# Kernel optimization log

Hardware: AMD Instinct MI355X
Metric: run time of the kernel (lower is better)

Reference implementation:

```python
import jax, jax.numpy as jnp
import numpy as np

V, H, T, B, S = 50000, 256, 32, 64, 512


def setup_inputs() -> dict:
    key = jax.random.key(0)
    ks = jax.random.split(key, 16)
    sc = 0.05
    def n(k, shape):
        return jax.random.normal(k, shape, dtype=jnp.float32) * sc
    return {
        "seq": jax.random.randint(ks[0], (B, S), 0, V),
        "mask": jnp.ones((B, S), dtype=jnp.int32),
        "labels": jax.random.randint(ks[1], (B, S), 0, T),
        "embedding": n(ks[2], (V, H)),
        "Wih_f": n(ks[3], (4 * H, H)), "Whh_f": n(ks[4], (4 * H, H)),
        "bih_f": n(ks[5], (4 * H,)), "bhh_f": n(ks[6], (4 * H,)),
        "Wih_b": n(ks[7], (4 * H, H)), "Whh_b": n(ks[8], (4 * H, H)),
        "bih_b": n(ks[9], (4 * H,)), "bhh_b": n(ks[10], (4 * H,)),
        "fcW": n(ks[11], (T, 2 * H)), "fcb": n(ks[12], (T,)),
        "start_trans": n(ks[13], (T,)), "end_trans": n(ks[14], (T,)),
        "trans": n(ks[15], (T, T)),
    }


def _lstm_dir(x, Wih, Whh, bih, bhh, reverse):
    # x: [S,B,H]; torch LSTM gate order i,f,g,o
    Bz, Hh = x.shape[1], Whh.shape[1]
    def step(carry, xt):
        h, c = carry
        g = xt @ Wih.T + h @ Whh.T + bih + bhh  # [B,4H]
        i, f, gg, o = jnp.split(g, 4, axis=-1)
        c = jax.nn.sigmoid(f) * c + jax.nn.sigmoid(i) * jnp.tanh(gg)
        h = jax.nn.sigmoid(o) * jnp.tanh(c)
        return (h, c), h
    init = (jnp.zeros((Bz, Hh), x.dtype), jnp.zeros((Bz, Hh), x.dtype))
    _, hs = jax.lax.scan(step, init, x, reverse=reverse)
    return hs


def _crf_llh(em, tags, mask, start, end, trans):
    # em [S,B,T], tags [S,B] int, mask [S,B] bool -> scalar sum log-likelihood
    Sx, Bx, Tx = em.shape
    barange = jnp.arange(Bx)
    em_sc = jnp.take_along_axis(em, tags[:, :, None], axis=2)[..., 0]  # [S,B]
    m = mask.astype(em.dtype)
    num = start[tags[0]] + em_sc[0]
    tr_sc = trans[tags[:-1], tags[1:]]  # [S-1,B]
    num = num + jnp.sum((tr_sc + em_sc[1:]) * m[1:], axis=0)
    seq_ends = jnp.sum(mask.astype(jnp.int32), axis=0) - 1
    last_tags = tags[seq_ends, barange]
    num = num + end[last_tags]
    # forward algorithm (log-partition)
    def step(score, em_m):
        em_t, m_t = em_m
        nxt = jax.nn.logsumexp(score[:, :, None] + trans[None], axis=1) + em_t
        return jnp.where(m_t[:, None], nxt, score), None
    score0 = start[None] + em[0]
    score, _ = jax.lax.scan(step, score0, (em[1:], mask[1:]))
    den = jax.nn.logsumexp(score + end[None], axis=1)
    return jnp.sum(num - den)


def _viterbi(em, mask, start, end, trans):
    Sx, Bx, Tx = em.shape
    def step(score, em_m):
        em_t, m_t = em_m
        cand = score[:, :, None] + trans[None]  # [B,T_prev,T_cur]
        idx = jnp.argmax(cand, axis=1)
        nxt = jnp.max(cand, axis=1) + em_t
        idx = jnp.where(m_t[:, None], idx, jnp.arange(Tx)[None])
        return jnp.where(m_t[:, None], nxt, score), idx
    score0 = start[None] + em[0]
    score, hist = jax.lax.scan(step, score0, (em[1:], mask[1:]))  # hist [S-1,B,T]
    last = jnp.argmax(score + end[None], axis=1)  # [B]
    barange = jnp.arange(Bx)
    def back(tag, idx_t):
        prev = idx_t[barange, tag]
        return prev, prev
    _, prevs = jax.lax.scan(back, last, hist, reverse=True)  # prevs[k] = tag at time k
    return jnp.concatenate([prevs, last[None]], axis=0)  # [S,B]


def reference(seq, mask, labels, embedding, Wih_f, Whh_f, bih_f, bhh_f,
              Wih_b, Whh_b, bih_b, bhh_b, fcW, fcb,
              start_trans, end_trans, trans):
    x = seq.T  # [S,B] time-major as in original
    emb = embedding[x]  # [S,B,H]
    hf = _lstm_dir(emb, Wih_f, Whh_f, bih_f, bhh_f, False)
    hb = _lstm_dir(emb, Wih_b, Whh_b, bih_b, bhh_b, True)
    out = jnp.concatenate([hf, hb], axis=-1)  # [S,B,2H]
    logits = out @ fcW.T + fcb  # [S,B,T]; dropout is identity at eval
    m = mask.T.astype(bool)  # [S,B]
    loss = -_crf_llh(logits, labels.T, m, start_trans, end_trans, trans)
    preds = _viterbi(logits, m, start_trans, end_trans, trans)  # [S,B]
    return preds.T, loss
```

## Files before the change

kernel.cpp:

```cpp
#include <hip/hip_runtime.h>
#include <stdint.h>

#define SS 512
#define BB 64
#define HH 256
#define TT 32

typedef __attribute__((ext_vector_type(8))) short bf16x8;
typedef __attribute__((ext_vector_type(4))) short short4v;
typedef __attribute__((ext_vector_type(4))) float f32x4;
typedef __attribute__((ext_vector_type(8))) int i32x8;
typedef __attribute__((ext_vector_type(4))) int i32x4;

__device__ __forceinline__ unsigned short f2bf(float f){
  unsigned u = __float_as_uint(f);
  unsigned r = (u + 0x7FFFu + ((u >> 16) & 1u)) >> 16;
  return (unsigned short)r;
}
__device__ __forceinline__ float bf2f(unsigned short s){
  return __uint_as_float(((unsigned)s) << 16);
}
__device__ __forceinline__ float sigm(float x){ return 1.0f/(1.0f+__expf(-x)); }
__device__ __forceinline__ float ftanh(float x){
  float e = __expf(2.f*x);
  return 1.f - 2.f/(e + 1.f);
}
__device__ __forceinline__ unsigned cvt4fp8(float a0, float a1, float a2, float a3){
  int d = __builtin_amdgcn_cvt_pk_fp8_f32(a0, a1, 0, false);
  d = __builtin_amdgcn_cvt_pk_fp8_f32(a2, a3, d, true);
  return (unsigned)d;
}
__device__ __forceinline__ unsigned short cvt2fp8(float a0, float a1){
  int d = __builtin_amdgcn_cvt_pk_fp8_f32(a0, a1, 0, false);
  return (unsigned short)(d & 0xFFFF);
}

__device__ __forceinline__ bf16x8 afrag(const unsigned short* A, int mt, int ktp, int nl, int kq){
  int m = mt*16 + nl;
  int sw = (m & 7) << 3;
  int kk = ktp*32 + kq*4;
  short4v lo = *(const short4v*)(A + (m << 8) + (kk ^ sw));
  short4v hi = *(const short4v*)(A + (m << 8) + ((kk + 16) ^ sw));
  bf16x8 r = {lo[0],lo[1],lo[2],lo[3],hi[0],hi[1],hi[2],hi[3]};
  return r;
}

__global__ __launch_bounds__(256,1) void k_xgemm(
    const int* __restrict__ seq, const float* __restrict__ emb,
    const float* __restrict__ Wih_f, const float* __restrict__ Wih_b,
    const float* __restrict__ bih_f, const float* __restrict__ bhh_f,
    const float* __restrict__ bih_b, const float* __restrict__ bhh_b,
    unsigned short* __restrict__ gx)
{
  __shared__ __align__(16) unsigned short A_l[128*256];
  __shared__ __align__(16) unsigned short B_l[64*256];

  const int tid = threadIdx.x;
  const int lane = tid & 63, w = tid >> 6;
  const int nl = lane & 15, kq = lane >> 4;
  const int pbase = blockIdx.x * 128;
  const int dir = blockIdx.y;
  const float* Wih  = dir ? Wih_b : Wih_f;
  const float* bihd = dir ? bih_b : bih_f;
  const float* bhhd = dir ? bhh_b : bhh_f;

#pragma unroll
  for (int i = 0; i < 16; ++i){
    int c = tid + i*256;
    int m = c >> 5, k8 = c & 31;
    int p = pbase + m, t = p >> 6, b = p & 63;
    int er = seq[b*SS + t];
    const float* s = emb + (size_t)er*HH + k8*8;
    float4 x0 = *(const float4*)s, x1 = *(const float4*)(s+4);
    union { unsigned short u[8]; uint4 v; } o;
    o.u[0]=f2bf(x0.x); o.u[1]=f2bf(x0.y); o.u[2]=f2bf(x0.z); o.u[3]=f2bf(x0.w);
    o.u[4]=f2bf(x1.x); o.u[5]=f2bf(x1.y); o.u[6]=f2bf(x1.z); o.u[7]=f2bf(x1.w);
    *(uint4*)&A_l[(m << 8) + ((k8*8) ^ ((m & 7) << 3))] = o.v;
  }

  for (int nb = 0; nb < 16; ++nb){
    __syncthreads();
#pragma unroll
    for (int i = 0; i < 8; ++i){
      int c = tid + i*256;
      int m = c >> 5, k8 = c & 31;
      const float* s = Wih + (size_t)(nb*64 + m)*HH + k8*8;
      float4 x0 = *(const float4*)s, x1 = *(const float4*)(s+4);
      union { unsigned short u[8]; uint4 v; } o;
      o.u[0]=f2bf(x0.x); o.u[1]=f2bf(x0.y); o.u[2]=f2bf(x0.z); o.u[3]=f2bf(x0.w);
      o.u[4]=f2bf(x1.x); o.u[5]=f2bf(x1.y); o.u[6]=f2bf(x1.z); o.u[7]=f2bf(x1.w);
      *(uint4*)&B_l[(m << 8) + ((k8*8) ^ ((m & 7) << 3))] = o.v;
    }
    __syncthreads();

    f32x4 acc[2][4];
#pragma unroll
    for (int mt = 0; mt < 2; ++mt)
#pragma unroll
      for (int nt = 0; nt < 4; ++nt) acc[mt][nt] = (f32x4){0.f,0.f,0.f,0.f};

#pragma unroll
    for (int kt = 0; kt < 8; ++kt){
      bf16x8 a0 = afrag(A_l, w*2+0, kt, nl, kq);
      bf16x8 a1 = afrag(A_l, w*2+1, kt, nl, kq);
#pragma unroll
      for (int nt = 0; nt < 4; ++nt){
        bf16x8 bv = afrag(B_l, nt, kt, nl, kq);
        acc[0][nt] = __builtin_amdgcn_mfma_f32_16x16x32_bf16(a0, bv, acc[0][nt], 0,0,0);
        acc[1][nt] = __builtin_amdgcn_mfma_f32_16x16x32_bf16(a1, bv, acc[1][nt], 0,0,0);
      }
    }

#pragma unroll
    for (int mt = 0; mt < 2; ++mt)
#pragma unroll
      for (int nt = 0; nt < 4; ++nt){
        int p0 = pbase + w*32 + mt*16 + kq*4;
        int t = p0 >> 6, b0 = p0 & 63;
        int col = nb*64 + nt*16 + nl;
        float bs = bihd[col] + bhhd[col];
        union { unsigned short u[4]; uint2 v; } o;
        o.u[0]=f2bf(acc[mt][nt][0] + bs); o.u[1]=f2bf(acc[mt][nt][1] + bs);
        o.u[2]=f2bf(acc[mt][nt][2] + bs); o.u[3]=f2bf(acc[mt][nt][3] + bs);
        *(uint2*)(gx + ((size_t)(dir*16 + (b0 >> 2))*SS + t)*4096 + col*4) = o.v;
      }
  }
}

#define WSC 64.0f
#define HSC 16.0f
#define ISC (1.0f/(WSC*HSC))

__global__ __launch_bounds__(1024,1) void k_lstm(
    const unsigned short* __restrict__ gx,
    const float* __restrict__ Whh_f, const float* __restrict__ Whh_b,
    unsigned short* __restrict__ hf, unsigned short* __restrict__ hb)
{
  __shared__ __align__(16) unsigned char h8[2][16][272];
  __shared__ __align__(16) float xch[16][4][16][4];

  const int tid  = threadIdx.x;
  const int lane = tid & 63;
  const int w    = tid >> 6;
  const int nl   = lane & 15;
  const int kq   = lane >> 4;
  const int dir  = blockIdx.x >> 4;
  const int bg   = blockIdx.x & 15;

  const float* Whh = dir ? Whh_b : Whh_f;
  unsigned short* hbuf = dir ? hb : hf;
  const unsigned short* gxd = gx + (size_t)(dir*16 + bg)*SS*4096;

  i32x8 wB[4][2];
#pragma unroll
  for (int g = 0; g < 4; ++g)
#pragma unroll
    for (int inst = 0; inst < 2; ++inst){
      int ncol = g*256 + w*16 + nl;
      i32x8 bfrag;
#pragma unroll
      for (int d = 0; d < 8; ++d){
        int k0 = inst*128 + kq*32 + d*4;
        float4 v = *(const float4*)(Whh + (size_t)ncol*HH + k0);
        bfrag[d] = (int)cvt4fp8(v.x*WSC, v.y*WSC, v.z*WSC, v.w*WSC);
      }
      wB[g][inst] = bfrag;
    }

  const int cc = w*16 + nl;

  for (int i = tid; i < 2176; i += 1024) ((unsigned*)h8)[i] = 0;
  __syncthreads();

  float c0 = 0.f;

  const int aoff = nl*272 + kq*32;
  const int woff = kq*272 + w*16 + nl;
  const ptrdiff_t gstep = dir ? -4096 : 4096;
  const unsigned short* gbase = gxd + (size_t)(dir ? (SS-1) : 0)*4096 + cc*4 + kq;
  unsigned short* hstore = hbuf + (size_t)(dir ? (SS-1) : 1)*BB*HH + (size_t)(bg*4 + kq)*HH + cc;
  const ptrdiff_t hstep = (dir ? -(ptrdiff_t)1 : (ptrdiff_t)1)*BB*HH;

  unsigned short gxc[4], gxn[4];
#pragma unroll
  for (int g = 0; g < 4; ++g) gxc[g] = gbase[g*1024];

  for (int s = 0; s < SS; ++s){
    const unsigned short* gnext = (s + 1 < SS) ? (gbase + gstep) : gbase;
#pragma unroll
    for (int g = 0; g < 4; ++g) gxn[g] = gnext[g*1024];

    const unsigned char* tp8 = &h8[s & 1][0][0] + aoff;
    i32x8 af0, af1;
    {
      i32x4 lo = *(const i32x4*)(tp8);
      i32x4 hi = *(const i32x4*)(tp8 + 16);
      af0 = (i32x8){lo[0],lo[1],lo[2],lo[3],hi[0],hi[1],hi[2],hi[3]};
      i32x4 lo2 = *(const i32x4*)(tp8 + 128);
      i32x4 hi2 = *(const i32x4*)(tp8 + 144);
      af1 = (i32x8){lo2[0],lo2[1],lo2[2],lo2[3],hi2[0],hi2[1],hi2[2],hi2[3]};
    }

    f32x4 acc[4];
#pragma unroll
    for (int g = 0; g < 4; ++g) acc[g] = (f32x4){0.f,0.f,0.f,0.f};

#pragma unroll
    for (int g = 0; g < 4; ++g)
      acc[g] = __builtin_amdgcn_mfma_scale_f32_16x16x128_f8f6f4(
                 af0, wB[g][0], acc[g], 0, 0, 0, 0x7F7F7F7F, 0, 0x7F7F7F7F);
#pragma unroll
    for (int g = 0; g < 4; ++g)
      acc[g] = __builtin_amdgcn_mfma_scale_f32_16x16x128_f8f6f4(
                 af1, wB[g][1], acc[g], 0, 0, 0, 0x7F7F7F7F, 0, 0x7F7F7F7F);

    if (kq == 0){
#pragma unroll
      for (int g = 0; g < 4; ++g)
        *(f32x4*)&xch[w][g][nl][0] = acc[g];
    }
    asm volatile("s_waitcnt lgkmcnt(0)" ::: "memory");

    {
      float i_ = xch[w][0][nl][kq]*ISC + bf2f(gxc[0]);
      float f_ = xch[w][1][nl][kq]*ISC + bf2f(gxc[1]);
      float g_ = xch[w][2][nl][kq]*ISC + bf2f(gxc[2]);
      float o_ = xch[w][3][nl][kq]*ISC + bf2f(gxc[3]);
      float cn = sigm(f_)*c0 + sigm(i_)*ftanh(g_);
      c0 = cn;
      float h = sigm(o_)*ftanh(cn);

      float s1 = __shfl_xor(h, 1);
      unsigned short p01 = cvt2fp8(h*HSC, s1*HSC);
      unsigned p23 = __shfl_xor((unsigned)p01, 2);
      if ((nl & 3) == 0){
        unsigned word = (unsigned)p01 | (p23 << 16);
        *(unsigned*)(&h8[(s + 1) & 1][0][0] + woff) = word;
      }
      if (!(nl & 1)){
        unsigned hv;
        asm volatile("v_cvt_pk_bf16_f32 %0, %1, %2" : "=v"(hv) : "v"(h), "v"(s1));
        *(unsigned*)hstore = hv;
      }
    }

#pragma unroll
    for (int g = 0; g < 4; ++g) gxc[g] = gxn[g];
    gbase = gnext;
    hstore += hstep;

    asm volatile("s_waitcnt lgkmcnt(0)" ::: "memory");
    __builtin_amdgcn_s_barrier();
    asm volatile("" ::: "memory");
  }
}

__global__ __launch_bounds__(256,1) void k_fc(
    const unsigned short* __restrict__ hf, const unsigned short* __restrict__ hb,
    const float* __restrict__ fcW, const float* __restrict__ fcb,
    float* __restrict__ logits)
{
  __shared__ unsigned short Bs[32][516];
  __shared__ unsigned short Ah[4][32][260];
  __shared__ float fcb_s[32];
  const int tid = threadIdx.x;
  for (int i = tid; i < 32*512; i += 256){
    int tg = i >> 9, k = i & 511;
    Bs[tg][k] = f2bf(fcW[tg*512 + k]);
  }
  if (tid < 32) fcb_s[tid] = fcb[tid];
  __syncthreads();

  const int lane = tid & 63, w = tid >> 6;
  const int nl = lane & 15, kq = lane >> 4;
  const int pbase = blockIdx.x * 128;

  f32x4 acc[2][2];
#pragma unroll
  for (int mt = 0; mt < 2; ++mt)
#pragma unroll
    for (int nt = 0; nt < 2; ++nt) acc[mt][nt] = (f32x4){0.f,0.f,0.f,0.f};

  for (int half = 0; half < 2; ++half){
    for (int rr = 0; rr < 32; ++rr){
      int p = pbase + w*32 + rr;
      int t = p >> 6, b = p & 63;
      const unsigned short* src = half ? (hb + (size_t)(t*BB + b)*HH)
                                       : (hf + (size_t)((t+1)*BB + b)*HH);
      *(uint2*)&Ah[w][rr][lane*4] = *(const uint2*)(src + lane*4);
    }
#pragma unroll
    for (int kt = 0; kt < 8; ++kt){
      int kl = kt*32 + kq*4;
      bf16x8 a[2];
#pragma unroll
      for (int mt = 0; mt < 2; ++mt){
        const unsigned short* ar = &Ah[w][mt*16 + nl][kl];
        short4v lo = *(const short4v*)ar;
        short4v hi = *(const short4v*)(ar + 16);
        bf16x8 f = {lo[0],lo[1],lo[2],lo[3],hi[0],hi[1],hi[2],hi[3]};
        a[mt] = f;
      }
#pragma unroll
      for (int nt = 0; nt < 2; ++nt){
        const unsigned short* br = &Bs[nt*16 + nl][half*256 + kl];
        short4v lo = *(const short4v*)br;
        short4v hi = *(const short4v*)(br + 16);
        bf16x8 bv = {lo[0],lo[1],lo[2],lo[3],hi[0],hi[1],hi[2],hi[3]};
        acc[0][nt] = __builtin_amdgcn_mfma_f32_16x16x32_bf16(a[0], bv, acc[0][nt], 0,0,0);
        acc[1][nt] = __builtin_amdgcn_mfma_f32_16x16x32_bf16(a[1], bv, acc[1][nt], 0,0,0);
      }
    }
  }
#pragma unroll
  for (int mt = 0; mt < 2; ++mt)
#pragma unroll
    for (int nt = 0; nt < 2; ++nt)
#pragma unroll
      for (int r = 0; r < 4; ++r){
        int p = pbase + w*32 + mt*16 + kq*4 + r;
        int tg = nt*16 + nl;
        logits[(size_t)p*TT + tg] = acc[mt][nt][r] + fcb_s[tg];
      }
}

__global__ void k_crf(const float* __restrict__ logits, const int* __restrict__ mask,
                      const int* __restrict__ labels,
                      const float* __restrict__ start, const float* __restrict__ endt,
                      const float* __restrict__ trans,
                      float* __restrict__ den, float* __restrict__ num,
                      float* __restrict__ preds)
{
  __shared__ float tr[1024];
  __shared__ unsigned char vh_l[4][SS-1][32];
  const int tid = threadIdx.x;
  const int role = blockIdx.x >> 4;
  const int bq   = blockIdx.x & 15;
  if (role != 2){
    for (int i = tid; i < 1024; i += 256) tr[i] = trans[i];
    __syncthreads();
  }
  const int lane = tid & 63, w = tid >> 6;
  const int b = bq*4 + w;
  const int grp = lane >> 5, tp = lane & 31;

  if (role == 0){
    float score = start[tp] + logits[(size_t)b*TT + tp];
    float em_c = logits[(size_t)(BB + b)*TT + tp];
    int   mk_c = mask[b*SS + 1];
    for (int s = 1; s < SS; ++s){
      int sn = (s + 1 < SS) ? s + 1 : s;
      float em_n = logits[(size_t)(sn*BB + b)*TT + tp];
      int   mk_n = mask[b*SS + sn];
      float m = -1e30f;
#pragma unroll
      for (int jj = 0; jj < 16; ++jj){
        int j = grp*16 + jj;
        float v = __shfl(score, j) + tr[j*32 + tp];
        m = fmaxf(m, v);
      }
      m = fmaxf(m, __shfl_xor(m, 32));
      float ssum = 0.f;
#pragma unroll
      for (int jj = 0; jj < 16; ++jj){
        int j = grp*16 + jj;
        float v = __shfl(score, j) + tr[j*32 + tp];
        ssum += __expf(v - m);
      }
      ssum += __shfl_xor(ssum, 32);
      float ns = m + __logf(ssum) + em_c;
      score = mk_c ? ns : score;
      em_c = em_n; mk_c = mk_n;
    }
    float v = score + endt[tp];
    float mm = v;
    for (int d = 1; d < 32; d <<= 1) mm = fmaxf(mm, __shfl_xor(mm, d));
    float se = __expf(v - mm);
    for (int d = 1; d < 32; d <<= 1) se += __shfl_xor(se, d);
    if (lane == 0) den[b] = mm + __logf(se);
  } else if (role == 1){
    float score = start[tp] + logits[(size_t)b*TT + tp];
    float em_c = logits[(size_t)(BB + b)*TT + tp];
    int   mk_c = mask[b*SS + 1];
    for (int s = 1; s < SS; ++s){
      int sn = (s + 1 < SS) ? s + 1 : s;
      float em_n = logits[(size_t)(sn*BB + b)*TT + tp];
      int   mk_n = mask[b*SS + sn];
      float m = -1e30f; int am = 0;
#pragma unroll
      for (int jj = 0; jj < 16; ++jj){
        int j = grp*16 + jj;
        float v = __shfl(score, j) + tr[j*32 + tp];
        if (v > m){ m = v; am = j; }
      }
      float om = __shfl_xor(m, 32); int oam = __shfl_xor(am, 32);
      if (om > m || (om == m && oam < am)){ m = om; am = oam; }
      float ns = m + em_c;
      int idx = mk_c ? am : tp;
      if (grp == 0) vh_l[w][s-1][tp] = (unsigned char)idx;
      score = mk_c ? ns : score;
      em_c = em_n; mk_c = mk_n;
    }
    float v = score + endt[tp]; int a = tp;
    for (int d = 1; d < 32; d <<= 1){
      float ov = __shfl_xor(v, d); int oa = __shfl_xor(a, d);
      if (ov > v || (ov == v && oa < a)){ v = ov; a = oa; }
    }
    int tag = __shfl(a, 0);
    if (lane == 0) preds[(size_t)b*SS + SS - 1] = (float)tag;
    for (int s = SS - 1; s >= 1; --s){
      int rv = vh_l[w][s-1][tp];
      int pv = __shfl(rv, tag);
      if (lane == 0) preds[(size_t)b*SS + s - 1] = (float)pv;
      tag = pv;
    }
  } else {
    float acc = 0.f; int mcnt = 0;
    for (int s = lane; s < SS; s += 64){
      int mk = mask[b*SS + s];
      mcnt += mk;
      if (s >= 1){
        int tg = labels[b*SS + s], tpp = labels[b*SS + s - 1];
        float v = trans[tpp*32 + tg] + logits[(size_t)(s*BB + b)*TT + tg];
        acc += mk ? v : 0.f;
      }
    }
    for (int d = 1; d < 64; d <<= 1){ acc += __shfl_xor(acc, d); mcnt += __shfl_xor(mcnt, d); }
    if (lane == 0){
      int t0 = labels[b*SS];
      int tl = labels[b*SS + (mcnt - 1)];
      num[b] = start[t0] + logits[(size_t)b*TT + t0] + acc + endt[tl];
    }
  }
}

__global__ void k_loss(const float* __restrict__ num, const float* __restrict__ den,
                       float* __restrict__ out)
{
  int l = threadIdx.x;
  float v = num[l] - den[l];
  for (int d = 1; d < 64; d <<= 1) v += __shfl_xor(v, d);
  if (l == 0) out[BB*SS] = -v;
}

extern "C" void kernel_launch(void* const* d_in, const int* in_sizes, int n_in,
                              void* d_out, int out_size, void* d_ws, size_t ws_size,
                              hipStream_t stream)
{
  const int*   seq       = (const int*)  d_in[0];
  const int*   mask      = (const int*)  d_in[1];
  const int*   labels    = (const int*)  d_in[2];
  const float* embedding = (const float*)d_in[3];
  const float* Wih_f     = (const float*)d_in[4];
  const float* Whh_f     = (const float*)d_in[5];
  const float* bih_f     = (const float*)d_in[6];
  const float* bhh_f     = (const float*)d_in[7];
  const float* Wih_b     = (const float*)d_in[8];
  const float* Whh_b     = (const float*)d_in[9];
  const float* bih_b     = (const float*)d_in[10];
  const float* bhh_b     = (const float*)d_in[11];
  const float* fcW       = (const float*)d_in[12];
  const float* fcb       = (const float*)d_in[13];
  const float* start_t   = (const float*)d_in[14];
  const float* end_t     = (const float*)d_in[15];
  const float* trans     = (const float*)d_in[16];

  char* ws = (char*)d_ws;
  size_t off = 0;
  unsigned short* gxb = (unsigned short*)(ws + off); off += (size_t)2*SS*1024*64*2;
  unsigned short* hf  = (unsigned short*)(ws + off); off += (size_t)(SS+1)*BB*HH*2;
  unsigned short* hb  = (unsigned short*)(ws + off); off += (size_t)(SS+1)*BB*HH*2;
  float*          lgt = (float*)(ws + off);          off += (size_t)SS*BB*TT*4;
  float*          den = (float*)(ws + off);          off += 256;
  float*          num = (float*)(ws + off);          off += 256;

  k_xgemm<<<dim3(256,2), 256, 0, stream>>>(seq, embedding, Wih_f, Wih_b,
                                           bih_f, bhh_f, bih_b, bhh_b, gxb);
  k_lstm<<<32, 1024, 0, stream>>>(gxb, Whh_f, Whh_b, hf, hb);
  k_fc<<<256, 256, 0, stream>>>(hf, hb, fcW, fcb, lgt);
  k_crf<<<48, 256, 0, stream>>>(lgt, mask, labels, start_t, end_t, trans, den, num, (float*)d_out);
  k_loss<<<1, 64, 0, stream>>>(num, den, (float*)d_out);
}
```

Before: 1.385 ms.

## Fuse input GEMM and LSTM recurrence into one kernel with flag-based overlap

Merges the input-projection GEMM and the recurrent LSTM into a single launch. The first 32 blocks run the recurrence, and the remaining blocks compute gate pre-activations in time order, publishing per-tile completion flags through atomics. LSTM blocks poll these flags before consuming each timestep, so the serial recurrence can start while the GEMM is still running instead of waiting for a full separate kernel. This relies on the GEMM blocks actually being scheduled alongside the resident LSTM blocks. It also adds atomic loads, polling with a guard counter, and an extra memset launch.

```diff
diff --git a/kernel.cpp b/kernel.cpp
--- a/kernel.cpp
+++ b/kernel.cpp
@@ -45,111 +45,114 @@
   return r;
 }
 
-__global__ __launch_bounds__(256,1) void k_xgemm(
+#define WSC 64.0f
+#define HSC 16.0f
+#define ISC (1.0f/(WSC*HSC))
+
+__global__ __launch_bounds__(1024,1) void k_fused(
     const int* __restrict__ seq, const float* __restrict__ emb,
     const float* __restrict__ Wih_f, const float* __restrict__ Wih_b,
     const float* __restrict__ bih_f, const float* __restrict__ bhh_f,
     const float* __restrict__ bih_b, const float* __restrict__ bhh_b,
-    unsigned short* __restrict__ gx)
+    const float* __restrict__ Whh_f, const float* __restrict__ Whh_b,
+    unsigned short* __restrict__ gx,
+    unsigned short* __restrict__ hf, unsigned short* __restrict__ hb,
+    unsigned int* flags)
 {
-  __shared__ __align__(16) unsigned short A_l[128*256];
-  __shared__ __align__(16) unsigned short B_l[64*256];
-
-  const int tid = threadIdx.x;
-  const int lane = tid & 63, w = tid >> 6;
-  const int nl = lane & 15, kq = lane >> 4;
-  const int pbase = blockIdx.x * 128;
-  const int dir = blockIdx.y;
-  const float* Wih  = dir ? Wih_b : Wih_f;
-  const float* bihd = dir ? bih_b : bih_f;
-  const float* bhhd = dir ? bhh_b : bhh_f;
-
-#pragma unroll
-  for (int i = 0; i < 16; ++i){
-    int c = tid + i*256;
-    int m = c >> 5, k8 = c & 31;
-    int p = pbase + m, t = p >> 6, b = p & 63;
-    int er = seq[b*SS + t];
-    const float* s = emb + (size_t)er*HH + k8*8;
-    float4 x0 = *(const float4*)s, x1 = *(const float4*)(s+4);
-    union { unsigned short u[8]; uint4 v; } o;
-    o.u[0]=f2bf(x0.x); o.u[1]=f2bf(x0.y); o.u[2]=f2bf(x0.z); o.u[3]=f2bf(x0.w);
-    o.u[4]=f2bf(x1.x); o.u[5]=f2bf(x1.y); o.u[6]=f2bf(x1.z); o.u[7]=f2bf(x1.w);
-    *(uint4*)&A_l[(m << 8) + ((k8*8) ^ ((m & 7) << 3))] = o.v;
-  }
-
-  for (int nb = 0; nb < 16; ++nb){
-    __syncthreads();
-#pragma unroll
-    for (int i = 0; i < 8; ++i){
-      int c = tid + i*256;
-      int m = c >> 5, k8 = c & 31;
-      const float* s = Wih + (size_t)(nb*64 + m)*HH + k8*8;
-      float4 x0 = *(const float4*)s, x1 = *(const float4*)(s+4);
-      union { unsigned short u[8]; uint4 v; } o;
-      o.u[0]=f2bf(x0.x); o.u[1]=f2bf(x0.y); o.u[2]=f2bf(x0.z); o.u[3]=f2bf(x0.w);
-      o.u[4]=f2bf(x1.x); o.u[5]=f2bf(x1.y); o.u[6]=f2bf(x1.z); o.u[7]=f2bf(x1.w);
-      *(uint4*)&B_l[(m << 8) + ((k8*8) ^ ((m & 7) << 3))] = o.v;
-    }
-    __syncthreads();
-
-    f32x4 acc[2][4];
-#pragma unroll
-    for (int mt = 0; mt < 2; ++mt)
-#pragma unroll
-      for (int nt = 0; nt < 4; ++nt) acc[mt][nt] = (f32x4){0.f,0.f,0.f,0.f};
-
-#pragma unroll
-    for (int kt = 0; kt < 8; ++kt){
-      bf16x8 a0 = afrag(A_l, w*2+0, kt, nl, kq);
-      bf16x8 a1 = afrag(A_l, w*2+1, kt, nl, kq);
-#pragma unroll
-      for (int nt = 0; nt < 4; ++nt){
-        bf16x8 bv = afrag(B_l, nt, kt, nl, kq);
-        acc[0][nt] = __builtin_amdgcn_mfma_f32_16x16x32_bf16(a0, bv, acc[0][nt], 0,0,0);
-        acc[1][nt] = __builtin_amdgcn_mfma_f32_16x16x32_bf16(a1, bv, acc[1][nt], 0,0,0);
-      }
-    }
-
-#pragma unroll
-    for (int mt = 0; mt < 2; ++mt)
-#pragma unroll
-      for (int nt = 0; nt < 4; ++nt){
-        int p0 = pbase + w*32 + mt*16 + kq*4;
-        int t = p0 >> 6, b0 = p0 & 63;
-        int col = nb*64 + nt*16 + nl;
-        float bs = bihd[col] + bhhd[col];
-        union { unsigned short u[4]; uint2 v; } o;
-        o.u[0]=f2bf(acc[mt][nt][0] + bs); o.u[1]=f2bf(acc[mt][nt][1] + bs);
-        o.u[2]=f2bf(acc[mt][nt][2] + bs); o.u[3]=f2bf(acc[mt][nt][3] + bs);
-        *(uint2*)(gx + ((size_t)(dir*16 + (b0 >> 2))*SS + t)*4096 + col*4) = o.v;
-      }
-  }
-}
-
-#define WSC 64.0f
-#define HSC 16.0f
-#define ISC (1.0f/(WSC*HSC))
-
-__global__ __launch_bounds__(1024,1) void k_lstm(
-    const unsigned short* __restrict__ gx,
-    const float* __restrict__ Whh_f, const float* __restrict__ Whh_b,
-    unsigned short* __restrict__ hf, unsigned short* __restrict__ hb)
-{
-  __shared__ __align__(16) unsigned char h8[2][16][272];
-  __shared__ __align__(16) float xch[16][4][16][4];
-
+  __shared__ __align__(16) unsigned char smem[98304];
   const int tid  = threadIdx.x;
   const int lane = tid & 63;
   const int w    = tid >> 6;
   const int nl   = lane & 15;
   const int kq   = lane >> 4;
-  const int dir  = blockIdx.x >> 4;
-  const int bg   = blockIdx.x & 15;
-
+
+  if (blockIdx.x >= 32){
+    unsigned short* A_l = (unsigned short*)smem;
+    unsigned short* B_l = (unsigned short*)(smem + 65536);
+    const int e    = blockIdx.x - 32;
+    const int dir  = e & 1;
+    const int rest = e >> 1;
+    const int xi   = rest >> 2;
+    const int ch   = rest & 3;
+    const int xe   = dir ? (255 - xi) : xi;
+    const int pbase = xe * 128;
+    const float* Wih  = dir ? Wih_b : Wih_f;
+    const float* bihd = dir ? bih_b : bih_f;
+    const float* bhhd = dir ? bhh_b : bhh_f;
+    const int m8 = w & 7, nh = w >> 3;
+
+#pragma unroll
+    for (int i = 0; i < 4; ++i){
+      int c = tid + i*1024;
+      int m = c >> 5, k8 = c & 31;
+      int p = pbase + m, t = p >> 6, b = p & 63;
+      int er = seq[b*SS + t];
+      const float* s = emb + (size_t)er*HH + k8*8;
+      float4 x0 = *(const float4*)s, x1 = *(const float4*)(s+4);
+      union { unsigned short u[8]; uint4 v; } o;
+      o.u[0]=f2bf(x0.x); o.u[1]=f2bf(x0.y); o.u[2]=f2bf(x0.z); o.u[3]=f2bf(x0.w);
+      o.u[4]=f2bf(x1.x); o.u[5]=f2bf(x1.y); o.u[6]=f2bf(x1.z); o.u[7]=f2bf(x1.w);
+      *(uint4*)&A_l[(m << 8) + ((k8*8) ^ ((m & 7) << 3))] = o.v;
+    }
+
+    for (int nq = 0; nq < 4; ++nq){
+      const int nb = ch*4 + nq;
+      __syncthreads();
+#pragma unroll
+      for (int i = 0; i < 2; ++i){
+        int c = tid + i*1024;
+        int m = c >> 5, k8 = c & 31;
+        const float* s = Wih + (size_t)(nb*64 + m)*HH + k8*8;
+        float4 x0 = *(const float4*)s, x1 = *(const float4*)(s+4);
+        union { unsigned short u[8]; uint4 v; } o;
+        o.u[0]=f2bf(x0.x); o.u[1]=f2bf(x0.y); o.u[2]=f2bf(x0.z); o.u[3]=f2bf(x0.w);
+        o.u[4]=f2bf(x1.x); o.u[5]=f2bf(x1.y); o.u[6]=f2bf(x1.z); o.u[7]=f2bf(x1.w);
+        *(uint4*)&B_l[(m << 8) + ((k8*8) ^ ((m & 7) << 3))] = o.v;
+      }
+      __syncthreads();
+
+      f32x4 acc0 = {0.f,0.f,0.f,0.f}, acc1 = acc0;
+#pragma unroll
+      for (int kt = 0; kt < 8; ++kt){
+        bf16x8 a0 = afrag(A_l, m8, kt, nl, kq);
+        bf16x8 b0 = afrag(B_l, nh*2 + 0, kt, nl, kq);
+        bf16x8 b1 = afrag(B_l, nh*2 + 1, kt, nl, kq);
+        acc0 = __builtin_amdgcn_mfma_f32_16x16x32_bf16(a0, b0, acc0, 0,0,0);
+        acc1 = __builtin_amdgcn_mfma_f32_16x16x32_bf16(a0, b1, acc1, 0,0,0);
+      }
+
+      const int p0 = pbase + m8*16 + kq*4;
+      const int t = p0 >> 6, b0 = p0 & 63;
+#pragma unroll
+      for (int ntl = 0; ntl < 2; ++ntl){
+        int col = nb*64 + (nh*2 + ntl)*16 + nl;
+        float bs = bihd[col] + bhhd[col];
+        f32x4 A = ntl ? acc1 : acc0;
+        union { unsigned short u[4]; unsigned long long ll; } o;
+        o.u[0]=f2bf(A[0]+bs); o.u[1]=f2bf(A[1]+bs);
+        o.u[2]=f2bf(A[2]+bs); o.u[3]=f2bf(A[3]+bs);
+        __hip_atomic_store(
+          (unsigned long long*)(gx + ((size_t)(dir*16 + (b0 >> 2))*SS + t)*4096 + col*4),
+          o.ll, __ATOMIC_RELAXED, __HIP_MEMORY_SCOPE_AGENT);
+      }
+    }
+    __syncthreads();
+    if (tid == 0)
+      __hip_atomic_fetch_add(&flags[dir*256 + xe], 1u,
+                             __ATOMIC_RELAXED, __HIP_MEMORY_SCOPE_AGENT);
+    return;
+  }
+
+  unsigned char* h8b = smem;
+  float (*xch)[4][16][4] = (float(*)[4][16][4])(smem + 8704);
+  int* s_clear = (int*)(smem + 8704 + 16384);
+
+  const int dir = blockIdx.x >> 4;
+  const int bg  = blockIdx.x & 15;
   const float* Whh = dir ? Whh_b : Whh_f;
   unsigned short* hbuf = dir ? hb : hf;
   const unsigned short* gxd = gx + (size_t)(dir*16 + bg)*SS*4096;
+  const unsigned int* flg = flags + dir*256;
 
   i32x8 wB[4][2];
 #pragma unroll
@@ -168,29 +171,84 @@
     }
 
   const int cc = w*16 + nl;
-
-  for (int i = tid; i < 2176; i += 1024) ((unsigned*)h8)[i] = 0;
+  for (int i = tid; i < 2176; i += 1024) ((unsigned*)h8b)[i] = 0;
+  if (tid == 0) *s_clear = 0;
   __syncthreads();
 
   float c0 = 0.f;
-
   const int aoff = nl*272 + kq*32;
-  const int woff = kq*272 + w*16 + nl;
-  const ptrdiff_t gstep = dir ? -4096 : 4096;
-  const unsigned short* gbase = gxd + (size_t)(dir ? (SS-1) : 0)*4096 + cc*4 + kq;
-  unsigned short* hstore = hbuf + (size_t)(dir ? (SS-1) : 1)*BB*HH + (size_t)(bg*4 + kq)*HH + cc;
+  const int woff = kq*272 + cc;
+  const ptrdiff_t gustep = dir ? -2048 : 2048;
+  const unsigned* gubase =
+      (const unsigned*)(gxd + (size_t)(dir ? (SS-1) : 0)*4096 + cc*4 + (kq & ~1));
+  unsigned short* hstore =
+      hbuf + (size_t)(dir ? (SS-1) : 1)*BB*HH + (size_t)(bg*4 + kq)*HH + cc;
   const ptrdiff_t hstep = (dir ? -(ptrdiff_t)1 : (ptrdiff_t)1)*BB*HH;
+  const int hiSel = (kq & 1) ? 16 : 0;
+
+  int sclear_reg = 0;
+
+  {
+    if (tid == 0){
+      int c = 0, guard = 0;
+      while (c < 2){
+        int j = c >> 1;
+        int fi = dir ? (255 - j) : j;
+        if (__hip_atomic_load(&flg[fi], __ATOMIC_RELAXED, __HIP_MEMORY_SCOPE_AGENT) >= 4u) c += 2;
+        else { __builtin_amdgcn_s_sleep(8); if (++guard > (1 << 22)) { c = 2; break; } }
+      }
+      int lim = 64;
+      while (c < lim){
+        int j = c >> 1;
+        int fi = dir ? (255 - j) : j;
+        if (__hip_atomic_load(&flg[fi], __ATOMIC_RELAXED, __HIP_MEMORY_SCOPE_AGENT) >= 4u) c += 2;
+        else break;
+      }
+      *s_clear = c;
+    }
+    __syncthreads();
+    sclear_reg = *s_clear;
+  }
 
   unsigned short gxc[4], gxn[4];
 #pragma unroll
-  for (int g = 0; g < 4; ++g) gxc[g] = gbase[g*1024];
+  for (int g = 0; g < 4; ++g){
+    unsigned u = __hip_atomic_load(gubase + g*512, __ATOMIC_RELAXED, __HIP_MEMORY_SCOPE_AGENT);
+    gxc[g] = (unsigned short)(u >> hiSel);
+  }
 
   for (int s = 0; s < SS; ++s){
-    const unsigned short* gnext = (s + 1 < SS) ? (gbase + gstep) : gbase;
-#pragma unroll
-    for (int g = 0; g < 4; ++g) gxn[g] = gnext[g*1024];
-
-    const unsigned char* tp8 = &h8[s & 1][0][0] + aoff;
+    if (sclear_reg < s + 2){
+      if (tid == 0){
+        int c = *s_clear, guard = 0;
+        int tgt = s + 2; if (tgt > SS) tgt = SS;
+        while (c < tgt){
+          int j = c >> 1;
+          int fi = dir ? (255 - j) : j;
+          if (__hip_atomic_load(&flg[fi], __ATOMIC_RELAXED, __HIP_MEMORY_SCOPE_AGENT) >= 4u) c += 2;
+          else { __builtin_amdgcn_s_sleep(8); if (++guard > (1 << 22)) { c = tgt; break; } }
+        }
+        int lim = s + 64; if (lim > SS) lim = SS;
+        while (c < lim){
+          int j = c >> 1;
+          int fi = dir ? (255 - j) : j;
+          if (__hip_atomic_load(&flg[fi], __ATOMIC_RELAXED, __HIP_MEMORY_SCOPE_AGENT) >= 4u) c += 2;
+          else break;
+        }
+        *s_clear = c;
+      }
+      __syncthreads();
+      sclear_reg = *s_clear;
+    }
+
+    const unsigned* gun = (s + 1 < SS) ? (gubase + gustep) : gubase;
+#pragma unroll
+    for (int g = 0; g < 4; ++g){
+      unsigned u = __hip_atomic_load(gun + g*512, __ATOMIC_RELAXED, __HIP_MEMORY_SCOPE_AGENT);
+      gxn[g] = (unsigned short)(u >> hiSel);
+    }
+
+    const unsigned char* tp8 = h8b + (s & 1)*4352 + aoff;
     i32x8 af0, af1;
     {
       i32x4 lo = *(const i32x4*)(tp8);
@@ -204,7 +262,6 @@
     f32x4 acc[4];
 #pragma unroll
     for (int g = 0; g < 4; ++g) acc[g] = (f32x4){0.f,0.f,0.f,0.f};
-
 #pragma unroll
     for (int g = 0; g < 4; ++g)
       acc[g] = __builtin_amdgcn_mfma_scale_f32_16x16x128_f8f6f4(
@@ -235,7 +292,7 @@
       unsigned p23 = __shfl_xor((unsigned)p01, 2);
       if ((nl & 3) == 0){
         unsigned word = (unsigned)p01 | (p23 << 16);
-        *(unsigned*)(&h8[(s + 1) & 1][0][0] + woff) = word;
+        *(unsigned*)(h8b + ((s + 1) & 1)*4352 + woff) = word;
       }
       if (!(nl & 1)){
         unsigned hv;
@@ -246,7 +303,7 @@
 
 #pragma unroll
     for (int g = 0; g < 4; ++g) gxc[g] = gxn[g];
-    gbase = gnext;
+    gubase = gun;
     hstore += hstep;
 
     asm volatile("s_waitcnt lgkmcnt(0)" ::: "memory");
@@ -473,10 +530,13 @@
   float*          lgt = (float*)(ws + off);          off += (size_t)SS*BB*TT*4;
   float*          den = (float*)(ws + off);          off += 256;
   float*          num = (float*)(ws + off);          off += 256;
-
-  k_xgemm<<<dim3(256,2), 256, 0, stream>>>(seq, embedding, Wih_f, Wih_b,
-                                           bih_f, bhh_f, bih_b, bhh_b, gxb);
-  k_lstm<<<32, 1024, 0, stream>>>(gxb, Whh_f, Whh_b, hf, hb);
+  unsigned int*   flg = (unsigned int*)(ws + off);   off += 2*256*4;
+
+  hipMemsetAsync(flg, 0, 2*256*4, stream);
+
+  k_fused<<<2080, 1024, 0, stream>>>(seq, embedding, Wih_f, Wih_b,
+                                     bih_f, bhh_f, bih_b, bhh_b,
+                                     Whh_f, Whh_b, gxb, hf, hb, flg);
   k_fc<<<256, 256, 0, stream>>>(hf, hb, fcW, fcb, lgt);
   k_crf<<<48, 256, 0, stream>>>(lgt, mask, labels, start_t, end_t, trans, den, num, (float*)d_out);
   k_loss<<<1, 64, 0, stream>>>(num, den, (float*)d_out);
```

New measurement: 1.256 ms. 9.4% less time.
